# Kernel tuning notes

Measured on AMD Instinct MI355X. Metric: run time of the kernel, lower is better.

Reference implementation:

```python
import jax, jax.numpy as jnp
import numpy as np
from jax import lax

B, C, H, W = 16, 3, 256, 256
K = 3          # lbp kernel size (odd)
POOL = 3       # avg pool size (odd so shapes are preserved)
Q = 8          # quant_len


def _build_lbp_kernel():
    mid = K // 2
    idx_pairs = [((0, 0), (K - 1, K - 1)), ((0, mid), (K - 1, mid)),
                 ((0, K - 1), (K - 1, 0)), ((mid, K - 1), (mid, 0))]
    ks = []
    for a, b in idx_pairs:
        for pos in (a, b):
            k = np.zeros((C, K, K), np.float32)
            k[:, mid, mid] = 1.0
            k[:, pos[0], pos[1]] = -1.0
            ks.append(k)
    return jnp.asarray(np.stack(ks))  # [8, C, K, K]

LBP_KERNEL = _build_lbp_kernel()
# cartesian_prod(arange(Q), arange(Q)) -> first coord slowest (row-major)
IDXS = jnp.asarray(np.stack(np.meshgrid(np.arange(Q), np.arange(Q), indexing='ij'), -1)
                   .reshape(Q * Q, 2).astype(np.float32))  # [64, 2]


def _forward(x, w_expand, b_expand, w_conv, b_conv, w_final, b_final, clamp_low, clamp_high):
    b = x.shape[0]
    # avg_pool2d(kernel=POOL, stride=1, pad=POOL//2, count_include_pad=True)
    p = POOL // 2
    xp = jnp.pad(x, ((0, 0), (0, 0), (p, p), (p, p)))
    x = lax.reduce_window(xp, 0.0, lax.add, (1, 1, POOL, POOL), (1, 1, 1, 1), 'VALID') / (POOL * POOL)
    # 8-channel LBP difference conv, 'same' padding
    x = lax.conv_general_dilated(x, LBP_KERNEL, (1, 1), ((K // 2, K // 2), (K // 2, K // 2)),
                                 dimension_numbers=('NCHW', 'OIHW', 'NCHW'))  # [B,8,H,W]
    x = jnp.clip(x, clamp_low[0], clamp_high[0])
    b4 = b * 4
    v = x.reshape(b4, 2, H * W)                    # pairwise channels
    mn = v.min(-1)                                 # [b4,2]
    mx = v.max(-1)
    lev = mn[..., None] + (mx - mn)[..., None] * (jnp.arange(Q, dtype=v.dtype) / Q)  # [b4,2,Q]
    hi = jnp.concatenate([lev[..., 1:], mx[..., None]], -1)                          # [b4,2,Q]
    vq = v[:, :, None, :]                                                            # [b4,2,1,HW]
    # keep value if lev[l] <= v <= hi[l], else 0 (values equal to a boundary land in both bins)
    masked = jnp.where((vq >= lev[..., None]) & (vq <= hi[..., None]), vq, 0.0)      # [b4,2,Q,HW]
    # joint weighted histogram: sum_p v0[p in bin i] * v1[p in bin j]
    hist = jnp.einsum('bip,bjp->bij', masked[:, 0], masked[:, 1])                    # [b4,Q,Q]
    hist = (hist / jnp.sum(hist)).reshape(b4, Q * Q)
    feats = jnp.concatenate([jnp.broadcast_to(IDXS, (b4, Q * Q, 2)), hist[..., None]], -1)  # [b4,64,3]
    f = feats.reshape(b, 4, Q * Q, 3).transpose(0, 3, 1, 2)                          # [B,3,4,64]
    y = jax.nn.leaky_relu(jnp.einsum('bchw,oc->bohw', f, w_expand) + b_expand[None, :, None, None])
    y = y.transpose(0, 2, 3, 1)                                                      # [B,4,64,56]
    # torch nearest interpolate: src = floor(dst * in / out)
    h_in, w_in = y.shape[-2], y.shape[-1]
    rows = (jnp.arange(H) * h_in) // H
    cols = (jnp.arange(W) * w_in) // W
    y = y[:, :, rows][:, :, :, cols]                                                 # [B,4,H,W]
    # layer_norm over last two dims, no affine
    mean = y.mean((-2, -1), keepdims=True)
    var = ((y - mean) ** 2).mean((-2, -1), keepdims=True)
    y = (y - mean) / jnp.sqrt(var + 1e-5)
    y = jax.nn.leaky_relu(jnp.einsum('bchw,oc->bohw', y, w_conv) + b_conv[None, :, None, None])
    y = lax.conv_general_dilated(y, w_final, (1, 1), ((1, 1), (1, 1)),
                                 dimension_numbers=('NCHW', 'OIHW', 'NCHW')) + b_final[None, :, None, None]
    return jax.nn.leaky_relu(y)                                                      # [B,1,H,W]


def setup_inputs() -> dict:
    key = jax.random.key(0)
    ks = jax.random.split(key, 7)
    return {
        'x': jax.random.normal(ks[0], (B, C, H, W), jnp.float32),
        'w_expand': jax.random.normal(ks[1], (56, 3), jnp.float32) * 0.1,
        'b_expand': jax.random.normal(ks[2], (56,), jnp.float32) * 0.1,
        'w_conv': jax.random.normal(ks[3], (16, 4), jnp.float32) * 0.1,
        'b_conv': jax.random.normal(ks[4], (16,), jnp.float32) * 0.1,
        'w_final': jax.random.normal(ks[5], (1, 16, 3, 3), jnp.float32) * 0.1,
        'b_final': jax.random.normal(ks[6], (1,), jnp.float32) * 0.1,
        'clamp_low': jnp.full((1,), -150.0, jnp.float32),
        'clamp_high': jnp.full((1,), 150.0, jnp.float32),
    }


def reference(x, w_expand, b_expand, w_conv, b_conv, w_final, b_final, clamp_low, clamp_high):
    return _forward(x, w_expand, b_expand, w_conv, b_conv, w_final, b_final, clamp_low, clamp_high)
```

## Files before the change

kernel.cpp:

```cpp
#include <hip/hip_runtime.h>
#include <math.h>

#define NB   16
#define HW   65536
#define NCHM 32
#define NCHH 16

#define OFF_S    0
#define OFF_D    0
#define OFF_PH   1048576
#define OFF_PMN  1114112
#define OFF_PMX  1118208

__device__ __forceinline__ float leakyf(float v) { return v >= 0.f ? v : 0.01f * v; }

__global__ void k_box(const float* __restrict__ x, float* __restrict__ ws)
{
    __shared__ float t[18][20];
    int b  = blockIdx.z;
    int h0 = blockIdx.y * 16, w0 = blockIdx.x * 16;
    int tid = threadIdx.y * 16 + threadIdx.x;
    const float* xb = x + (size_t)b * 3 * HW;
    for (int i = tid; i < 18 * 18; i += 256) {
        int lh = i / 18, lw = i % 18;
        int gh = h0 - 1 + lh, gw = w0 - 1 + lw;
        float v = 0.f;
        if (gh >= 0 && gh < 256 && gw >= 0 && gw < 256) {
            int p = gh * 256 + gw;
            v = xb[p] + xb[HW + p] + xb[2 * HW + p];
        }
        t[lh][lw] = v;
    }
    __syncthreads();
    int ty = threadIdx.y, tx = threadIdx.x;
    float s = 0.f;
    #pragma unroll
    for (int dy = 0; dy < 3; ++dy)
        #pragma unroll
        for (int dx = 0; dx < 3; ++dx)
            s += t[ty + dy][tx + dx];
    ws[OFF_S + b * HW + (h0 + ty) * 256 + (w0 + tx)] = s / 9.0f;
}

__global__ void k_minmax_part(const float* __restrict__ clo, const float* __restrict__ chi,
                              float* ws)
{
    const int doy[8] = {-1, 1, -1, 1, -1, 1, 0, 0};
    const int dox[8] = {-1, 1,  0, 0,  1, -1, 1, -1};
    int b  = blockIdx.x / NCHM;
    int ch = blockIdx.x % NCHM;
    float lo = clo[0], hi = chi[0];
    const float* Sb = ws + OFF_S + b * HW;
    float vmn[8], vmx[8];
    #pragma unroll
    for (int o = 0; o < 8; ++o) { vmn[o] = 3.4e38f; vmx[o] = -3.4e38f; }
    int base = ch * (HW / NCHM);
    #pragma unroll
    for (int it = 0; it < (HW / NCHM) / 256; ++it) {
        int p = base + it * 256 + threadIdx.x;
        int h = p >> 8, w = p & 255;
        float sc = Sb[p];
        #pragma unroll
        for (int o = 0; o < 8; ++o) {
            int nh = h + doy[o], nw = w + dox[o];
            float off = ((unsigned)nh < 256u && (unsigned)nw < 256u) ? Sb[nh * 256 + nw] : 0.f;
            float v = fminf(fmaxf(sc - off, lo), hi);
            vmn[o] = fminf(vmn[o], v);
            vmx[o] = fmaxf(vmx[o], v);
        }
    }
    #pragma unroll
    for (int o = 0; o < 8; ++o) {
        #pragma unroll
        for (int m = 1; m < 64; m <<= 1) {
            vmn[o] = fminf(vmn[o], __shfl_xor(vmn[o], m));
            vmx[o] = fmaxf(vmx[o], __shfl_xor(vmx[o], m));
        }
    }
    __shared__ float smn[4][8], smx[4][8];
    int wid = threadIdx.x >> 6, lane = threadIdx.x & 63;
    if (lane == 0) {
        #pragma unroll
        for (int o = 0; o < 8; ++o) { smn[wid][o] = vmn[o]; smx[wid][o] = vmx[o]; }
    }
    __syncthreads();
    if (threadIdx.x < 8) {
        int o = threadIdx.x;
        float mn = fminf(fminf(smn[0][o], smn[1][o]), fminf(smn[2][o], smn[3][o]));
        float mx = fmaxf(fmaxf(smx[0][o], smx[1][o]), fmaxf(smx[2][o], smx[3][o]));
        ws[OFF_PMN + (b * 8 + o) * NCHM + ch] = mn;
        ws[OFF_PMX + (b * 8 + o) * NCHM + ch] = mx;
    }
}

__global__ void k_hist_part(const float* __restrict__ clo, const float* __restrict__ chi,
                            float* ws)
{
    __shared__ float lh[64 * 64];
    const int doy[8] = {-1, 1, -1, 1, -1, 1, 0, 0};
    const int dox[8] = {-1, 1,  0, 0,  1, -1, 1, -1};
    int bg = blockIdx.x / NCHH;
    int ch = blockIdx.x % NCHH;
    int b = bg >> 2, g = bg & 3;
    int dy0 = doy[2 * g], dx0 = dox[2 * g];
    int dy1 = doy[2 * g + 1], dx1 = dox[2 * g + 1];
    float mn0 = 3.4e38f, mx0 = -3.4e38f, mn1 = 3.4e38f, mx1 = -3.4e38f;
    {
        int c0 = (b * 8 + 2 * g) * NCHM, c1 = (b * 8 + 2 * g + 1) * NCHM;
        for (int c = 0; c < NCHM; ++c) {
            mn0 = fminf(mn0, ws[OFF_PMN + c0 + c]);
            mx0 = fmaxf(mx0, ws[OFF_PMX + c0 + c]);
            mn1 = fminf(mn1, ws[OFF_PMN + c1 + c]);
            mx1 = fmaxf(mx1, ws[OFF_PMX + c1 + c]);
        }
    }
    float r0 = mx0 - mn0, r1 = mx1 - mn1;
    float lev0[8], lev1[8];
    #pragma unroll
    for (int q = 0; q < 8; ++q) {
        lev0[q] = __fadd_rn(mn0, __fmul_rn(r0, (float)q * 0.125f));
        lev1[q] = __fadd_rn(mn1, __fmul_rn(r1, (float)q * 0.125f));
    }
    const float* Sb = ws + OFF_S + b * HW;
    for (int i = threadIdx.x; i < 4096; i += 256) lh[i] = 0.f;
    __syncthreads();
    int col = threadIdx.x & 63;
    float lo = clo[0], hi = chi[0];
    int base = ch * (HW / NCHH);
    #pragma unroll
    for (int it = 0; it < (HW / NCHH) / 256; ++it) {
        int p = base + it * 256 + threadIdx.x;
        int h = p >> 8, w = p & 255;
        float off0 = 0.f, off1 = 0.f;
        int nh = h + dy0, nw = w + dx0;
        if ((unsigned)nh < 256u && (unsigned)nw < 256u) off0 = Sb[nh * 256 + nw];
        nh = h + dy1; nw = w + dx1;
        if ((unsigned)nh < 256u && (unsigned)nw < 256u) off1 = Sb[nh * 256 + nw];
        float sc = Sb[p];
        float v0 = fminf(fmaxf(sc - off0, lo), hi);
        float v1 = fminf(fmaxf(sc - off1, lo), hi);
        int i0 = 0, j0 = 0;
        bool ilo = false, jlo = false;
        #pragma unroll
        for (int k = 1; k < 8; ++k) {
            i0 += (v0 >= lev0[k]); ilo |= (v0 == lev0[k]);
            j0 += (v1 >= lev1[k]); jlo |= (v1 == lev1[k]);
        }
        float prod = v0 * v1;
        atomicAdd(&lh[(i0 * 8 + j0) * 64 + col], prod);
        if (ilo)        atomicAdd(&lh[((i0 - 1) * 8 + j0) * 64 + col], prod);
        if (jlo)        atomicAdd(&lh[(i0 * 8 + (j0 - 1)) * 64 + col], prod);
        if (ilo && jlo) atomicAdd(&lh[((i0 - 1) * 8 + (j0 - 1)) * 64 + col], prod);
    }
    __syncthreads();
    if (threadIdx.x < 64) {
        int bin = threadIdx.x;
        float s = 0.f;
        for (int c = 0; c < 64; ++c) s += lh[bin * 64 + ((c + bin) & 63)];
        ws[OFF_PH + blockIdx.x * 64 + bin] = s;
    }
}

__global__ void __launch_bounds__(256) k_fuse(const float* __restrict__ we,
                                              const float* __restrict__ be,
                                              const float* __restrict__ wc,
                                              const float* __restrict__ bc,
                                              const float* __restrict__ wf,
                                              float* ws)
{
    __shared__ float shY[4 * 3584];
    __shared__ float sh_hist[256];
    __shared__ float sh_red[256];
    __shared__ float sh_wf[144];
    __shared__ float sh_we[168];
    __shared__ float sh_be[56];
    __shared__ float sh_wc[64];
    __shared__ float sh_bc[16];
    __shared__ float sh_stat[8];
    __shared__ float sw[4][8];
    __shared__ float sh_tot;
    int b = blockIdx.x;
    int tid = threadIdx.x;

    {
        int g = tid >> 6, bin = tid & 63;
        float s = 0.f;
        #pragma unroll
        for (int c = 0; c < NCHH; ++c)
            s += ws[OFF_PH + ((b * 4 + g) * NCHH + c) * 64 + bin];
        sh_hist[tid] = s;
    }
    {
        float s = 0.f;
        for (int k = 0; k < 256; ++k)
            s += ws[OFF_PH + k * 256 + tid];
        sh_red[tid] = s;
    }
    if (tid < 144) sh_wf[tid] = wf[tid];
    if (tid < 168) sh_we[tid] = we[tid];
    if (tid < 56)  sh_be[tid] = be[tid];
    if (tid < 64)  sh_wc[tid] = wc[tid];
    if (tid < 16)  sh_bc[tid] = bc[tid];
    __syncthreads();
    for (int k = 128; k > 0; k >>= 1) {
        if (tid < k) sh_red[tid] += sh_red[tid + k];
        __syncthreads();
    }
    if (tid == 0) sh_tot = sh_red[0];
    __syncthreads();
    float total = sh_tot;

    float ls[4] = {0.f, 0.f, 0.f, 0.f}, lss[4] = {0.f, 0.f, 0.f, 0.f};
    for (int it = 0; it < 56; ++it) {
        int g = it / 14;
        int rem = (it % 14) * 256 + tid;
        int q = rem / 56, o = rem % 56;
        float hv = sh_hist[g * 64 + q] / total;
        float y = sh_we[o * 3 + 0] * (float)(q >> 3)
                + sh_we[o * 3 + 1] * (float)(q & 7)
                + sh_we[o * 3 + 2] * hv + sh_be[o];
        y = leakyf(y);
        shY[g * 3584 + rem] = y;
        int cnt = ((32 * (o + 1) + 6) / 7) - ((32 * o + 6) / 7);
        float wgt = (float)(4 * cnt);
        ls[g]  += y * wgt;
        lss[g] += y * y * wgt;
    }
    #pragma unroll
    for (int g = 0; g < 4; ++g) {
        #pragma unroll
        for (int m = 1; m < 64; m <<= 1) {
            ls[g]  += __shfl_xor(ls[g], m);
            lss[g] += __shfl_xor(lss[g], m);
        }
    }
    int wid = tid >> 6, lane = tid & 63;
    if (lane == 0) {
        #pragma unroll
        for (int g = 0; g < 4; ++g) { sw[wid][g] = ls[g]; sw[wid][4 + g] = lss[g]; }
    }
    __syncthreads();
    if (tid < 4) {
        float m  = (sw[0][tid] + sw[1][tid] + sw[2][tid] + sw[3][tid]) / 65536.f;
        float sq = (sw[0][4 + tid] + sw[1][4 + tid] + sw[2][4 + tid] + sw[3][4 + tid]) / 65536.f;
        sh_stat[tid] = m;
        sh_stat[4 + tid] = 1.f / sqrtf(sq - m * m + 1e-5f);
    }
    __syncthreads();

    for (int it = 0; it < 14; ++it) {
        int rem = it * 256 + tid;
        float yn[4];
        #pragma unroll
        for (int g = 0; g < 4; ++g)
            yn[g] = (shY[g * 3584 + rem] - sh_stat[g]) * sh_stat[4 + g];
        float d[9] = {0.f, 0.f, 0.f, 0.f, 0.f, 0.f, 0.f, 0.f, 0.f};
        #pragma unroll
        for (int c = 0; c < 16; ++c) {
            float z = sh_bc[c];
            #pragma unroll
            for (int g = 0; g < 4; ++g) z += sh_wc[c * 4 + g] * yn[g];
            z = leakyf(z);
            #pragma unroll
            for (int t = 0; t < 9; ++t) d[t] += z * sh_wf[c * 9 + t];
        }
        #pragma unroll
        for (int t = 0; t < 9; ++t)
            ws[OFF_D + (b * 9 + t) * 3584 + rem] = d[t];
    }
}

__global__ void __launch_bounds__(256) k_final(const float* __restrict__ ws,
                                               const float* __restrict__ bf,
                                               float* __restrict__ out)
{
    int pix = blockIdx.x * 256 + threadIdx.x;
    int w = pix & 255, h = (pix >> 8) & 255, b = pix >> 16;
    const float* Db = ws + OFF_D + b * 9 * 3584;
    float acc = 0.f;
    #pragma unroll
    for (int kh = 0; kh < 3; ++kh) {
        int h2 = h + kh - 1;
        if ((unsigned)h2 > 255u) continue;
        int qr = h2 >> 2;
        #pragma unroll
        for (int kw = 0; kw < 3; ++kw) {
            int w2 = w + kw - 1;
            if ((unsigned)w2 > 255u) continue;
            int oc = (w2 * 7) >> 5;
            acc += Db[(kh * 3 + kw) * 3584 + qr * 56 + oc];
        }
    }
    out[pix] = leakyf(acc + bf[0]);
}

extern "C" void kernel_launch(void* const* d_in, const int* in_sizes, int n_in,
                              void* d_out, int out_size, void* d_ws, size_t ws_size,
                              hipStream_t stream)
{
    const float* x   = (const float*)d_in[0];
    const float* we  = (const float*)d_in[1];
    const float* be  = (const float*)d_in[2];
    const float* wc  = (const float*)d_in[3];
    const float* bc  = (const float*)d_in[4];
    const float* wf  = (const float*)d_in[5];
    const float* bfi = (const float*)d_in[6];
    const float* clo = (const float*)d_in[7];
    const float* chi = (const float*)d_in[8];
    float* out = (float*)d_out;
    float* ws  = (float*)d_ws;

    dim3 blk(16, 16);
    dim3 grd(16, 16, NB);
    k_box<<<grd, blk, 0, stream>>>(x, ws);
    k_minmax_part<<<NB * NCHM, 256, 0, stream>>>(clo, chi, ws);
    k_hist_part<<<64 * NCHH, 256, 0, stream>>>(clo, chi, ws);
    k_fuse<<<NB, 256, 0, stream>>>(we, be, wc, bc, wf, ws);
    k_final<<<4096, 256, 0, stream>>>(ws, bfi, out);
}
```

Before: 159.8 us.

## Fuse box filter with LBP min/max partial reduction into one tiled kernel

Merges the 3x3 box-average kernel and the per-channel min/max partial kernel into a single kernel that computes a 32x32 tile plus a one-pixel halo of the pooled image in shared memory. The min/max is then taken from shared memory instead of re-reading the pooled image from global memory, which also removes one launch. The hist kernel reduces the 64 partials per channel with wave shuffles, and the fuse kernel's total-sum read is vectorized with float4. In exchange the halo is recomputed redundantly per tile and shared-memory use per block goes up.

```diff
diff --git a/kernel.cpp b/kernel.cpp
--- a/kernel.cpp
+++ b/kernel.cpp
@@ -3,67 +3,72 @@
 
 #define NB   16
 #define HW   65536
-#define NCHM 32
 #define NCHH 16
 
 #define OFF_S    0
 #define OFF_D    0
 #define OFF_PH   1048576
 #define OFF_PMN  1114112
-#define OFF_PMX  1118208
+#define OFF_PMX  1122304
 
 __device__ __forceinline__ float leakyf(float v) { return v >= 0.f ? v : 0.01f * v; }
 
-__global__ void k_box(const float* __restrict__ x, float* __restrict__ ws)
-{
-    __shared__ float t[18][20];
-    int b  = blockIdx.z;
-    int h0 = blockIdx.y * 16, w0 = blockIdx.x * 16;
-    int tid = threadIdx.y * 16 + threadIdx.x;
+__global__ void __launch_bounds__(256) k_boxmm(const float* __restrict__ x,
+                                               const float* __restrict__ clo,
+                                               const float* __restrict__ chi,
+                                               float* __restrict__ ws)
+{
+    __shared__ float inp[36][37];
+    __shared__ float S[34][36];
+    const int doy[8] = {-1, 1, -1, 1, -1, 1, 0, 0};
+    const int dox[8] = {-1, 1,  0, 0,  1, -1, 1, -1};
+    int b = blockIdx.z;
+    int h0 = blockIdx.y * 32, w0 = blockIdx.x * 32;
+    int tid = threadIdx.x;
     const float* xb = x + (size_t)b * 3 * HW;
-    for (int i = tid; i < 18 * 18; i += 256) {
-        int lh = i / 18, lw = i % 18;
-        int gh = h0 - 1 + lh, gw = w0 - 1 + lw;
+    for (int i = tid; i < 36 * 36; i += 256) {
+        int lh = i / 36, lw = i % 36;
+        int gh = h0 - 2 + lh, gw = w0 - 2 + lw;
         float v = 0.f;
-        if (gh >= 0 && gh < 256 && gw >= 0 && gw < 256) {
+        if ((unsigned)gh < 256u && (unsigned)gw < 256u) {
             int p = gh * 256 + gw;
             v = xb[p] + xb[HW + p] + xb[2 * HW + p];
         }
-        t[lh][lw] = v;
-    }
-    __syncthreads();
-    int ty = threadIdx.y, tx = threadIdx.x;
-    float s = 0.f;
-    #pragma unroll
-    for (int dy = 0; dy < 3; ++dy)
-        #pragma unroll
-        for (int dx = 0; dx < 3; ++dx)
-            s += t[ty + dy][tx + dx];
-    ws[OFF_S + b * HW + (h0 + ty) * 256 + (w0 + tx)] = s / 9.0f;
-}
-
-__global__ void k_minmax_part(const float* __restrict__ clo, const float* __restrict__ chi,
-                              float* ws)
-{
-    const int doy[8] = {-1, 1, -1, 1, -1, 1, 0, 0};
-    const int dox[8] = {-1, 1,  0, 0,  1, -1, 1, -1};
-    int b  = blockIdx.x / NCHM;
-    int ch = blockIdx.x % NCHM;
+        inp[lh][lw] = v;
+    }
+    __syncthreads();
+    for (int i = tid; i < 34 * 34; i += 256) {
+        int lh = i / 34, lw = i % 34;
+        float s = 0.f;
+        #pragma unroll
+        for (int dy = 0; dy < 3; ++dy)
+            #pragma unroll
+            for (int dx = 0; dx < 3; ++dx)
+                s += inp[lh + dy][lw + dx];
+        S[lh][lw] = s / 9.0f;
+    }
+    __syncthreads();
+    #pragma unroll
+    for (int i = 0; i < 4; ++i) {
+        int idx = i * 256 + tid;
+        int r = idx >> 5, c = idx & 31;
+        ws[OFF_S + b * HW + (h0 + r) * 256 + (w0 + c)] = S[r + 1][c + 1];
+    }
     float lo = clo[0], hi = chi[0];
-    const float* Sb = ws + OFF_S + b * HW;
     float vmn[8], vmx[8];
     #pragma unroll
     for (int o = 0; o < 8; ++o) { vmn[o] = 3.4e38f; vmx[o] = -3.4e38f; }
-    int base = ch * (HW / NCHM);
-    #pragma unroll
-    for (int it = 0; it < (HW / NCHM) / 256; ++it) {
-        int p = base + it * 256 + threadIdx.x;
-        int h = p >> 8, w = p & 255;
-        float sc = Sb[p];
+    #pragma unroll
+    for (int i = 0; i < 4; ++i) {
+        int idx = i * 256 + tid;
+        int r = idx >> 5, c = idx & 31;
+        int gh = h0 + r, gw = w0 + c;
+        float sc = S[r + 1][c + 1];
         #pragma unroll
         for (int o = 0; o < 8; ++o) {
-            int nh = h + doy[o], nw = w + dox[o];
-            float off = ((unsigned)nh < 256u && (unsigned)nw < 256u) ? Sb[nh * 256 + nw] : 0.f;
+            int nh = gh + doy[o], nw = gw + dox[o];
+            float off = ((unsigned)nh < 256u && (unsigned)nw < 256u)
+                        ? S[r + 1 + doy[o]][c + 1 + dox[o]] : 0.f;
             float v = fminf(fmaxf(sc - off, lo), hi);
             vmn[o] = fminf(vmn[o], v);
             vmx[o] = fmaxf(vmx[o], v);
@@ -78,25 +83,28 @@
         }
     }
     __shared__ float smn[4][8], smx[4][8];
-    int wid = threadIdx.x >> 6, lane = threadIdx.x & 63;
+    int wid = tid >> 6, lane = tid & 63;
     if (lane == 0) {
         #pragma unroll
         for (int o = 0; o < 8; ++o) { smn[wid][o] = vmn[o]; smx[wid][o] = vmx[o]; }
     }
     __syncthreads();
-    if (threadIdx.x < 8) {
-        int o = threadIdx.x;
+    if (tid < 8) {
+        int o = tid;
+        int tile = blockIdx.y * 8 + blockIdx.x;
         float mn = fminf(fminf(smn[0][o], smn[1][o]), fminf(smn[2][o], smn[3][o]));
         float mx = fmaxf(fmaxf(smx[0][o], smx[1][o]), fmaxf(smx[2][o], smx[3][o]));
-        ws[OFF_PMN + (b * 8 + o) * NCHM + ch] = mn;
-        ws[OFF_PMX + (b * 8 + o) * NCHM + ch] = mx;
-    }
-}
-
-__global__ void k_hist_part(const float* __restrict__ clo, const float* __restrict__ chi,
-                            float* ws)
+        ws[OFF_PMN + (b * 8 + o) * 64 + tile] = mn;
+        ws[OFF_PMX + (b * 8 + o) * 64 + tile] = mx;
+    }
+}
+
+__global__ void __launch_bounds__(256) k_hist_part(const float* __restrict__ clo,
+                                                   const float* __restrict__ chi,
+                                                   float* ws)
 {
     __shared__ float lh[64 * 64];
+    __shared__ float sred[4];
     const int doy[8] = {-1, 1, -1, 1, -1, 1, 0, 0};
     const int dox[8] = {-1, 1,  0, 0,  1, -1, 1, -1};
     int bg = blockIdx.x / NCHH;
@@ -104,16 +112,26 @@
     int b = bg >> 2, g = bg & 3;
     int dy0 = doy[2 * g], dx0 = dox[2 * g];
     int dy1 = doy[2 * g + 1], dx1 = dox[2 * g + 1];
-    float mn0 = 3.4e38f, mx0 = -3.4e38f, mn1 = 3.4e38f, mx1 = -3.4e38f;
+    int tid = threadIdx.x;
+    int warp = tid >> 6, lane = tid & 63;
     {
-        int c0 = (b * 8 + 2 * g) * NCHM, c1 = (b * 8 + 2 * g + 1) * NCHM;
-        for (int c = 0; c < NCHM; ++c) {
-            mn0 = fminf(mn0, ws[OFF_PMN + c0 + c]);
-            mx0 = fmaxf(mx0, ws[OFF_PMX + c0 + c]);
-            mn1 = fminf(mn1, ws[OFF_PMN + c1 + c]);
-            mx1 = fmaxf(mx1, ws[OFF_PMX + c1 + c]);
-        }
-    }
+        int c0 = (b * 8 + 2 * g) * 64, c1 = (b * 8 + 2 * g + 1) * 64;
+        float v;
+        if      (warp == 0) v = ws[OFF_PMN + c0 + lane];
+        else if (warp == 1) v = ws[OFF_PMX + c0 + lane];
+        else if (warp == 2) v = ws[OFF_PMN + c1 + lane];
+        else                v = ws[OFF_PMX + c1 + lane];
+        bool isMin = (warp & 1) == 0;
+        #pragma unroll
+        for (int m = 1; m < 64; m <<= 1) {
+            float o = __shfl_xor(v, m);
+            v = isMin ? fminf(v, o) : fmaxf(v, o);
+        }
+        if (lane == 0) sred[warp] = v;
+    }
+    for (int i = tid; i < 4096; i += 256) lh[i] = 0.f;
+    __syncthreads();
+    float mn0 = sred[0], mx0 = sred[1], mn1 = sred[2], mx1 = sred[3];
     float r0 = mx0 - mn0, r1 = mx1 - mn1;
     float lev0[8], lev1[8];
     #pragma unroll
@@ -122,14 +140,12 @@
         lev1[q] = __fadd_rn(mn1, __fmul_rn(r1, (float)q * 0.125f));
     }
     const float* Sb = ws + OFF_S + b * HW;
-    for (int i = threadIdx.x; i < 4096; i += 256) lh[i] = 0.f;
-    __syncthreads();
-    int col = threadIdx.x & 63;
+    int col = tid & 63;
     float lo = clo[0], hi = chi[0];
     int base = ch * (HW / NCHH);
     #pragma unroll
     for (int it = 0; it < (HW / NCHH) / 256; ++it) {
-        int p = base + it * 256 + threadIdx.x;
+        int p = base + it * 256 + tid;
         int h = p >> 8, w = p & 255;
         float off0 = 0.f, off1 = 0.f;
         int nh = h + dy0, nw = w + dx0;
@@ -153,8 +169,8 @@
         if (ilo && jlo) atomicAdd(&lh[((i0 - 1) * 8 + (j0 - 1)) * 64 + col], prod);
     }
     __syncthreads();
-    if (threadIdx.x < 64) {
-        int bin = threadIdx.x;
+    if (tid < 64) {
+        int bin = tid;
         float s = 0.f;
         for (int c = 0; c < 64; ++c) s += lh[bin * 64 + ((c + bin) & 63)];
         ws[OFF_PH + blockIdx.x * 64 + bin] = s;
@@ -191,9 +207,12 @@
         sh_hist[tid] = s;
     }
     {
+        const float4* ph4 = (const float4*)(ws + OFF_PH);
         float s = 0.f;
-        for (int k = 0; k < 256; ++k)
-            s += ws[OFF_PH + k * 256 + tid];
+        for (int k = 0; k < 64; ++k) {
+            float4 v = ph4[k * 256 + tid];
+            s += v.x + v.y + v.z + v.w;
+        }
         sh_red[tid] = s;
     }
     if (tid < 144) sh_wf[tid] = wf[tid];
@@ -310,10 +329,7 @@
     float* out = (float*)d_out;
     float* ws  = (float*)d_ws;
 
-    dim3 blk(16, 16);
-    dim3 grd(16, 16, NB);
-    k_box<<<grd, blk, 0, stream>>>(x, ws);
-    k_minmax_part<<<NB * NCHM, 256, 0, stream>>>(clo, chi, ws);
+    k_boxmm<<<dim3(8, 8, NB), 256, 0, stream>>>(x, clo, chi, ws);
     k_hist_part<<<64 * NCHH, 256, 0, stream>>>(clo, chi, ws);
     k_fuse<<<NB, 256, 0, stream>>>(we, be, wc, bc, wf, ws);
     k_final<<<4096, 256, 0, stream>>>(ws, bfi, out);
```

After: 153.2 us. -4.1%, faster.
